# Kernel optimization log

Measured on AMD Instinct MI355X. Metric: run time of the kernel, lower is better.

## Reference

```python
import math
import jax, jax.numpy as jnp
import numpy as np

B, T, C = 2, 2048, 1024
H, HKV, HD = 16, 4, 64  # n_head, n_kv_head, head_dim
G = H // HKV            # GQA groups
WS = 1024               # sliding window size
GATE_CH = 32


def setup_inputs() -> dict:
    key = jax.random.key(0)
    ks = jax.random.split(key, 8)
    x = jax.random.normal(ks[0], (B, T, C), dtype=jnp.float32)
    ve = jax.random.normal(ks[1], (B, T, HKV * HD), dtype=jnp.float32)
    # realistic RoPE tables: half head_dim frequencies
    d = HD // 2
    inv_freq = 1.0 / (10000.0 ** (jnp.arange(d, dtype=jnp.float32) / d))
    angles = jnp.arange(T, dtype=jnp.float32)[:, None] * inv_freq[None, :]  # (T, d)
    cos = jnp.cos(angles)[None, :, None, :]  # (1, T, 1, d)
    sin = jnp.sin(angles)[None, :, None, :]
    s = 0.02
    Wq = s * jax.random.normal(ks[2], (C, H * HD), dtype=jnp.float32)
    Wk = s * jax.random.normal(ks[3], (C, HKV * HD), dtype=jnp.float32)
    Wv = s * jax.random.normal(ks[4], (C, HKV * HD), dtype=jnp.float32)
    Wproj = s * jax.random.normal(ks[5], (C, C), dtype=jnp.float32)
    Wg = s * jax.random.normal(ks[6], (GATE_CH, HKV), dtype=jnp.float32)
    return {"x": x, "ve": ve, "cos": cos, "sin": sin,
            "Wq": Wq, "Wk": Wk, "Wv": Wv, "Wproj": Wproj, "Wg": Wg, "ws": WS}


def _rope(u, cos, sin):
    d = u.shape[-1] // 2
    u1, u2 = u[..., :d], u[..., d:]
    return jnp.concatenate([u1 * cos + u2 * sin, -u1 * sin + u2 * cos], axis=-1)


def _rmsnorm(u):
    eps = jnp.finfo(u.dtype).eps
    return u * jax.lax.rsqrt(jnp.mean(u * u, axis=-1, keepdims=True) + eps)


def reference(x, ve, cos, sin, Wq, Wk, Wv, Wproj, Wg, ws):
    b, t, c = x.shape
    q = (x @ Wq).reshape(b, t, H, HD)
    k = (x @ Wk).reshape(b, t, HKV, HD)
    v = (x @ Wv).reshape(b, t, HKV, HD)
    # value-embedding gate: 2*sigmoid over first 32 channels of x
    gate = 2.0 * jax.nn.sigmoid(x[..., :GATE_CH] @ Wg)  # (b, t, HKV)
    v = v + gate[..., None] * ve.reshape(b, t, HKV, HD)
    q = _rmsnorm(_rope(q, cos, sin))
    k = _rmsnorm(_rope(k, cos, sin))
    # GQA: view q as (b, t, HKV, G, HD), contract against shared k/v per kv-head
    qg = q.reshape(b, t, HKV, G, HD)
    scale = 1.0 / math.sqrt(HD)
    scores = jnp.einsum('bqhgd,bkhd->bhgqk', qg, k) * scale  # (b, HKV, G, t, t)
    pos = jnp.arange(t)
    # key j attends iff i - ws + 1 <= j <= i (sliding causal window)
    mask = (pos[None, :] >= pos[:, None] - ws + 1) & (pos[None, :] <= pos[:, None])
    scores = jnp.where(mask[None, None, None], scores, -jnp.inf)
    attn = jax.nn.softmax(scores, axis=-1)
    y = jnp.einsum('bhgqk,bkhd->bqhgd', attn, v).reshape(b, t, H * HD)
    return y @ Wproj
```

## Files before the change

kernel.cpp:

```cpp
#include <hip/hip_runtime.h>
#include <hip/hip_bf16.h>

#define Bq 2
#define Tq 2048
#define Cq 1024
#define Hq 16
#define HKVq 4
#define HDq 64
#define Gq 4
#define WSq 1024
#define GATE_CHq 32

typedef __attribute__((ext_vector_type(8))) short short8;
typedef __attribute__((ext_vector_type(4))) float f32x4;
typedef __attribute__((ext_vector_type(2))) unsigned int u32x2;
typedef unsigned int u32;
typedef unsigned short u16;

#if __has_builtin(__builtin_amdgcn_exp2f)
#define EXP2(x) __builtin_amdgcn_exp2f(x)
#else
#define EXP2(x) exp2f(x)
#endif

__device__ __forceinline__ u16 f2bf(float f) {
  u32 u = __float_as_uint(f);
  u32 r = (u + 0x7FFFu + ((u >> 16) & 1u)) >> 16;
  return (u16)r;
}
__device__ __forceinline__ float bf2f(u16 u) {
  return __uint_as_float(((u32)u) << 16);
}

__device__ __forceinline__ void gl_lds16(const u16* g, u16* l) {
  __builtin_amdgcn_global_load_lds(
      (const u32 __attribute__((address_space(1)))*)g,
      (u32 __attribute__((address_space(3)))*)l, 16, 0, 0);
}

__global__ __launch_bounds__(256) void qkv_gemm_fused(
    const u16* __restrict__ A, const u16* __restrict__ Bt,
    const float* __restrict__ ve, const float* __restrict__ cosp,
    const float* __restrict__ sinp, const float* __restrict__ gatebuf,
    u16* __restrict__ Qb, u16* __restrict__ Kb, u16* __restrict__ Vtb) {
  __shared__ __attribute__((aligned(16))) u16 As[64 * 64];
  __shared__ __attribute__((aligned(16))) u16 Bs[128 * 64];

  const int bx = blockIdx.x;
  const int bm0 = blockIdx.y * 64, bn0 = bx * 128;
  const int tid = threadIdx.x;
  const int w = tid >> 6, lane = tid & 63;
  const int wm = (w >> 1) * 32, wn = (w & 1) * 64;
  const int quad = lane >> 4, l16 = lane & 15;
  const int K = 1024;

  f32x4 acc[2][4];
#pragma unroll
  for (int mt = 0; mt < 2; mt++)
#pragma unroll
    for (int nt = 0; nt < 4; nt++) acc[mt][nt] = (f32x4){0.f, 0.f, 0.f, 0.f};

  int goffA[2], goffB[4];
#pragma unroll
  for (int i = 0; i < 2; i++) {
    int s = i * 256 + tid;
    int m = s >> 3, gp = s & 7;
    goffA[i] = m * K + (gp ^ (m & 7)) * 8;
  }
#pragma unroll
  for (int i = 0; i < 4; i++) {
    int s = i * 256 + tid;
    int m = s >> 3, gp = s & 7;
    goffB[i] = m * K + (gp ^ (m & 7)) * 8;
  }
  const u16* Ab = A + (long)bm0 * K;
  const u16* Bb = Bt + (long)bn0 * K;

  for (int k0 = 0; k0 < K; k0 += 64) {
    __syncthreads();
#pragma unroll
    for (int i = 0; i < 2; i++)
      gl_lds16(Ab + goffA[i] + k0, &As[(i * 256 + w * 64) * 8]);
#pragma unroll
    for (int i = 0; i < 4; i++)
      gl_lds16(Bb + goffB[i] + k0, &Bs[(i * 256 + w * 64) * 8]);
    __syncthreads();

#pragma unroll
    for (int ks = 0; ks < 2; ks++) {
      short8 af[2], bf[4];
#pragma unroll
      for (int mt = 0; mt < 2; mt++) {
        int ml = wm + mt * 16 + l16;
        af[mt] = *(const short8*)&As[ml * 64 + (((ks * 4 + quad) ^ (ml & 7)) * 8)];
      }
#pragma unroll
      for (int nt = 0; nt < 4; nt++) {
        int nl = wn + nt * 16 + l16;
        bf[nt] = *(const short8*)&Bs[nl * 64 + (((ks * 4 + quad) ^ (nl & 7)) * 8)];
      }
#pragma unroll
      for (int mt = 0; mt < 2; mt++)
#pragma unroll
        for (int nt = 0; nt < 4; nt++)
          acc[mt][nt] = __builtin_amdgcn_mfma_f32_16x16x32_bf16(
              af[mt], bf[nt], acc[mt][nt], 0, 0, 0);
    }
  }

  const int b = bm0 >> 11;
  const int tseq0 = (bm0 & 2047) + wm;

  if (bx < 10) {
    u16* Dst;
    if (bx < 8) {
      int hh = bx * 2 + (w & 1);
      int hkv = hh >> 2, g = hh & 3;
      Dst = Qb + ((long)((b * 4 + hkv) * 4 + g) * Tq) * 64;
    } else {
      int kk = (bx - 8) * 2 + (w & 1);
      Dst = Kb + ((long)(b * 4 + kk) * Tq) * 64;
    }
#pragma unroll
    for (int mt = 0; mt < 2; mt++) {
#pragma unroll
      for (int r = 0; r < 4; r++) {
        int t = tseq0 + mt * 16 + quad * 4 + r;
        float c0 = cosp[t * 32 + l16];
        float s0 = sinp[t * 32 + l16];
        float c1 = cosp[t * 32 + 16 + l16];
        float s1 = sinp[t * 32 + 16 + l16];
        float a0 = acc[mt][0][r], a1 = acc[mt][1][r];
        float a2 = acc[mt][2][r], a3 = acc[mt][3][r];
        float rp0 = a0 * c0 + a2 * s0;
        float rp1 = a1 * c1 + a3 * s1;
        float rp2 = a2 * c0 - a0 * s0;
        float rp3 = a3 * c1 - a1 * s1;
        float ss = rp0 * rp0 + rp1 * rp1 + rp2 * rp2 + rp3 * rp3;
        ss += __shfl_xor(ss, 1);
        ss += __shfl_xor(ss, 2);
        ss += __shfl_xor(ss, 4);
        ss += __shfl_xor(ss, 8);
        float sc = rsqrtf(ss * (1.f / 64.f) + 1.1920928955078125e-07f);
        u16* drow = Dst + (long)t * 64;
        drow[l16] = f2bf(rp0 * sc);
        drow[16 + l16] = f2bf(rp1 * sc);
        drow[32 + l16] = f2bf(rp2 * sc);
        drow[48 + l16] = f2bf(rp3 * sc);
      }
    }
  } else {
    int kk = (bx - 10) * 2 + (w & 1);
    u16* Dst = Vtb + ((long)(b * 4 + kk) * 64) * Tq;
#pragma unroll
    for (int mt = 0; mt < 2; mt++) {
      float vals[4][4];
#pragma unroll
      for (int r = 0; r < 4; r++) {
        int t = tseq0 + mt * 16 + quad * 4 + r;
        long bt = (long)b * Tq + t;
        float gv = gatebuf[bt * 4 + kk];
        const float* verow = ve + bt * 256 + kk * 64;
#pragma unroll
        for (int nt = 0; nt < 4; nt++)
          vals[nt][r] = acc[mt][nt][r] + gv * verow[nt * 16 + l16];
      }
      int t0m = tseq0 + mt * 16 + quad * 4;
#pragma unroll
      for (int nt = 0; nt < 4; nt++) {
        int d = nt * 16 + l16;
        union { short4 v; u16 u[4]; } p;
#pragma unroll
        for (int r = 0; r < 4; r++) p.u[r] = f2bf(vals[nt][r]);
        *(short4*)(Dst + (long)d * Tq + t0m) = p.v;
      }
    }
  }
}

__global__ __launch_bounds__(256) void gemm_proj(
    const u16* __restrict__ A, const u16* __restrict__ Bt,
    float* __restrict__ C, int M, int N, int K) {
  __shared__ __attribute__((aligned(16))) u16 As[64 * 64];
  __shared__ __attribute__((aligned(16))) u16 Bs[128 * 64];

  const int bm0 = blockIdx.y * 64, bn0 = blockIdx.x * 128;
  const int tid = threadIdx.x;
  const int w = tid >> 6, lane = tid & 63;
  const int wm = (w >> 1) * 32, wn = (w & 1) * 64;
  const int quad = lane >> 4, l16 = lane & 15;

  f32x4 acc[2][4];
#pragma unroll
  for (int mt = 0; mt < 2; mt++)
#pragma unroll
    for (int nt = 0; nt < 4; nt++) acc[mt][nt] = (f32x4){0.f, 0.f, 0.f, 0.f};

  int goffA[2], goffB[4];
#pragma unroll
  for (int i = 0; i < 2; i++) {
    int s = i * 256 + tid;
    int m = s >> 3, gp = s & 7;
    goffA[i] = m * K + (gp ^ (m & 7)) * 8;
  }
#pragma unroll
  for (int i = 0; i < 4; i++) {
    int s = i * 256 + tid;
    int m = s >> 3, gp = s & 7;
    goffB[i] = m * K + (gp ^ (m & 7)) * 8;
  }
  const u16* Ab = A + (long)bm0 * K;
  const u16* Bb = Bt + (long)bn0 * K;

  for (int k0 = 0; k0 < K; k0 += 64) {
    __syncthreads();
#pragma unroll
    for (int i = 0; i < 2; i++)
      gl_lds16(Ab + goffA[i] + k0, &As[(i * 256 + w * 64) * 8]);
#pragma unroll
    for (int i = 0; i < 4; i++)
      gl_lds16(Bb + goffB[i] + k0, &Bs[(i * 256 + w * 64) * 8]);
    __syncthreads();

#pragma unroll
    for (int ks = 0; ks < 2; ks++) {
      short8 af[2], bf[4];
#pragma unroll
      for (int mt = 0; mt < 2; mt++) {
        int ml = wm + mt * 16 + l16;
        af[mt] = *(const short8*)&As[ml * 64 + (((ks * 4 + quad) ^ (ml & 7)) * 8)];
      }
#pragma unroll
      for (int nt = 0; nt < 4; nt++) {
        int nl = wn + nt * 16 + l16;
        bf[nt] = *(const short8*)&Bs[nl * 64 + (((ks * 4 + quad) ^ (nl & 7)) * 8)];
      }
#pragma unroll
      for (int mt = 0; mt < 2; mt++)
#pragma unroll
        for (int nt = 0; nt < 4; nt++)
          acc[mt][nt] = __builtin_amdgcn_mfma_f32_16x16x32_bf16(
              af[mt], bf[nt], acc[mt][nt], 0, 0, 0);
    }
  }

#pragma unroll
  for (int mt = 0; mt < 2; mt++)
#pragma unroll
    for (int nt = 0; nt < 4; nt++) {
      int row0 = bm0 + wm + mt * 16 + quad * 4;
      int col = bn0 + wn + nt * 16 + l16;
#pragma unroll
      for (int r = 0; r < 4; r++)
        C[(long)(row0 + r) * N + col] = acc[mt][nt][r];
    }
}

__global__ __launch_bounds__(256) void prep(
    const float* __restrict__ x, u16* __restrict__ xb,
    const float* __restrict__ Wq, const float* __restrict__ Wk,
    const float* __restrict__ Wv, const float* __restrict__ Wproj,
    const float* __restrict__ Wg, u16* __restrict__ Dqkv,
    u16* __restrict__ Dproj, float* __restrict__ gatebuf) {
  __shared__ float tile[64][65];
  int bx = blockIdx.x;
  int tid = threadIdx.x;
  if (bx < 2048) {
    int i = (bx * 256 + tid) * 8;
    float4 a = *(const float4*)(x + i);
    float4 b = *(const float4*)(x + i + 4);
    union { short8 v; u16 u[8]; } o;
    o.u[0] = f2bf(a.x); o.u[1] = f2bf(a.y); o.u[2] = f2bf(a.z); o.u[3] = f2bf(a.w);
    o.u[4] = f2bf(b.x); o.u[5] = f2bf(b.y); o.u[6] = f2bf(b.z); o.u[7] = f2bf(b.w);
    *(short8*)(xb + i) = o.v;
    return;
  }
  if (bx >= 2688) {
    int p = (bx - 2688) * 256 + tid;
    int bt = p >> 2, kk = p & 3;
    const float* xr = x + (long)bt * Cq;
    float dot = 0.f;
#pragma unroll
    for (int i = 0; i < GATE_CHq; i++) dot += xr[i] * Wg[i * HKVq + kk];
    gatebuf[p] = 2.f / (1.f + expf(-dot));
    return;
  }
  int wb = bx - 2048;
  int obx = wb >> 4;
  int k0 = (wb & 15) * 64;
  const float* S;
  u16* Dst;
  int N, nb;
  if (obx < 16)      { S = Wq;    N = 1024; nb = obx;      Dst = Dqkv; }
  else if (obx < 20) { S = Wk;    N = 256;  nb = obx - 16; Dst = Dqkv + 1024 * 1024; }
  else if (obx < 24) { S = Wv;    N = 256;  nb = obx - 20; Dst = Dqkv + 1280 * 1024; }
  else               { S = Wproj; N = 1024; nb = obx - 24; Dst = Dproj; }
  int n0 = nb * 64;
#pragma unroll
  for (int i = 0; i < 16; i++) {
    int idx = i * 256 + tid;
    int kl = idx >> 6, nl = idx & 63;
    tile[kl][nl] = S[(long)(k0 + kl) * N + n0 + nl];
  }
  __syncthreads();
#pragma unroll
  for (int i = 0; i < 16; i++) {
    int idx = i * 256 + tid;
    int nl = idx >> 6, kl = idx & 63;
    Dst[(long)(n0 + nl) * 1024 + k0 + kl] = f2bf(tile[kl][nl]);
  }
}

#define CEXP 0.18033688011112042f
#define CEXP8 1.4426950408889634f

template <bool MASK>
__device__ __forceinline__ void attn_half(
    int k0h, int key_base, int vg_base, int q0, int quad, int l16,
    const u16* __restrict__ Ks, const u16* __restrict__ Vts,
    u32* __restrict__ myPs, const short8 (&QB)[2][2], f32x4 (&O)[2][4],
    float (&lsum)[2]) {
  f32x4 S4[4][2];
#pragma unroll
  for (int kt4 = 0; kt4 < 4; kt4++) {
    int key = key_base + kt4 * 16 + l16;
    short8 kb0 = *(const short8*)(&Ks[key * 64 + ((quad ^ (key & 7)) * 8)]);
    short8 kb1 = *(const short8*)(&Ks[key * 64 + (((4 + quad) ^ (key & 7)) * 8)]);
#pragma unroll
    for (int qj = 0; qj < 2; qj++) {
      f32x4 acc = (f32x4){0.f, 0.f, 0.f, 0.f};
      acc = __builtin_amdgcn_mfma_f32_16x16x32_bf16(kb0, QB[qj][0], acc, 0, 0, 0);
      acc = __builtin_amdgcn_mfma_f32_16x16x32_bf16(kb1, QB[qj][1], acc, 0, 0, 0);
      S4[kt4][qj] = acc;
    }
  }

#pragma unroll
  for (int kt4 = 0; kt4 < 4; kt4++)
#pragma unroll
    for (int qj = 0; qj < 2; qj++) {
      float Pv[4];
#pragma unroll
      for (int r = 0; r < 4; r++) {
        float sv = S4[kt4][qj][r];
        if (MASK) {
          int kpos = k0h + kt4 * 16 + quad * 4 + r;
          int qpos = q0 + qj * 16 + l16;
          bool valid = (kpos <= qpos) && (kpos >= qpos - (WSq - 1));
          sv = valid ? sv : -1e30f;
        }
        float p = EXP2(__builtin_fmaf(sv, CEXP, -CEXP8));
        Pv[r] = p;
        lsum[qj] += p;
      }
      u32x2 pk;
#pragma unroll
      for (int rp = 0; rp < 2; rp++) {
        u32 lo = __float_as_uint(Pv[2 * rp]) + 0x8000u;
        u32 hi = __float_as_uint(Pv[2 * rp + 1]) + 0x8000u;
        pk[rp] = __builtin_amdgcn_perm(hi, lo, 0x07060302u);
      }
      *(u32x2*)(&myPs[(qj * 16 + l16) * 36 + kt4 * 8 + quad * 2]) = pk;
    }

  short8 vb[4][2];
#pragma unroll
  for (int nt = 0; nt < 4; nt++) {
    int d = nt * 16 + l16;
    vb[nt][0] = *(const short8*)(&Vts[d * 128 + (((vg_base + quad) ^ (d & 7)) * 8)]);
    vb[nt][1] =
        *(const short8*)(&Vts[d * 128 + (((vg_base + 4 + quad) ^ (d & 7)) * 8)]);
  }

#pragma unroll
  for (int qj = 0; qj < 2; qj++) {
    const u32* prow = &myPs[(qj * 16 + l16) * 36];
    short8 pa0 = *(const short8*)(prow + quad * 4);
    short8 pa1 = *(const short8*)(prow + 16 + quad * 4);
#pragma unroll
    for (int nt = 0; nt < 4; nt++) {
      O[qj][nt] =
          __builtin_amdgcn_mfma_f32_16x16x32_bf16(pa0, vb[nt][0], O[qj][nt], 0, 0, 0);
      O[qj][nt] =
          __builtin_amdgcn_mfma_f32_16x16x32_bf16(pa1, vb[nt][1], O[qj][nt], 0, 0, 0);
    }
  }
}

__global__ __launch_bounds__(256, 2) void attn_mfma(
    const u16* __restrict__ Qb, const u16* __restrict__ Kb,
    const u16* __restrict__ Vtb, u16* __restrict__ Yb) {
  __shared__ __attribute__((aligned(16))) u16 Ks[128 * 64];
  __shared__ __attribute__((aligned(16))) u16 Vts[64 * 128];
  __shared__ __attribute__((aligned(16))) u32 Ps[4][2][32 * 36];

  int bid = blockIdx.x;
  int bh = bid & 7;
  int qt32 = bid >> 3;
  int hkv = bh & 3;
  int b = bh >> 2;
  int q0 = qt32 * 32;
  int tid = threadIdx.x;
  int g = tid >> 6;
  int lane = tid & 63;
  int quad = lane >> 4;
  int l16 = lane & 15;

  short8 QB[2][2];
#pragma unroll
  for (int qj = 0; qj < 2; qj++) {
    const u16* qb =
        Qb + ((long)((bh * 4 + g) * Tq + q0 + qj * 16 + l16)) * 64 + quad * 8;
    QB[qj][0] = *(const short8*)(qb);
    QB[qj][1] = *(const short8*)(qb + 32);
  }

  f32x4 O[2][4];
#pragma unroll
  for (int qj = 0; qj < 2; qj++)
#pragma unroll
    for (int nt = 0; nt < 4; nt++) O[qj][nt] = (f32x4){0.f, 0.f, 0.f, 0.f};
  float lsum[2] = {0.f, 0.f};

  int lo = q0 - (WSq - 1);
  int st = (lo < 0 ? 0 : lo) >> 7;
  int et = (q0 + 31) >> 7;

  const u16* Kbase = Kb + ((long)bh * Tq) * 64;
  const u16* Vbase = Vtb + ((long)bh * 64) * Tq;

  int rowoffK[4], rowoffV[4];
#pragma unroll
  for (int i = 0; i < 4; i++) {
    int s = i * 256 + tid;
    int kr = s >> 3, kgp = s & 7;
    rowoffK[i] = kr * 64 + (kgp ^ (kr & 7)) * 8;
    int d = s >> 4, vgp = s & 15;
    rowoffV[i] = d * Tq + (vgp ^ (d & 7)) * 8;
  }

  for (int kt = st; kt <= et; kt++) {
    int k0 = kt << 7;
    __syncthreads();
#pragma unroll
    for (int i = 0; i < 4; i++) {
      gl_lds16(Kbase + (long)k0 * 64 + rowoffK[i], &Ks[(i * 256 + g * 64) * 8]);
      gl_lds16(Vbase + k0 + rowoffV[i], &Vts[(i * 256 + g * 64) * 8]);
    }
    __syncthreads();

    bool needC = (k0 + 127 > q0);
    bool needW = (k0 < q0 - 992);
    if (needC || needW) {
      attn_half<true>(k0, 0, 0, q0, quad, l16, Ks, Vts, &Ps[g][0][0], QB, O, lsum);
      attn_half<true>(k0 + 64, 64, 8, q0, quad, l16, Ks, Vts, &Ps[g][1][0], QB,
                      O, lsum);
    } else {
      attn_half<false>(k0, 0, 0, q0, quad, l16, Ks, Vts, &Ps[g][0][0], QB, O,
                       lsum);
      attn_half<false>(k0 + 64, 64, 8, q0, quad, l16, Ks, Vts, &Ps[g][1][0], QB,
                       O, lsum);
    }
  }

#pragma unroll
  for (int qj = 0; qj < 2; qj++) {
    lsum[qj] += __shfl_xor(lsum[qj], 16);
    lsum[qj] += __shfl_xor(lsum[qj], 32);
  }

  int h = hkv * 4 + g;
#pragma unroll
  for (int qj = 0; qj < 2; qj++) {
    float invl[4];
#pragma unroll
    for (int r = 0; r < 4; r++) invl[r] = 1.f / __shfl(lsum[qj], quad * 4 + r);
#pragma unroll
    for (int nt = 0; nt < 4; nt++)
#pragma unroll
      for (int r = 0; r < 4; r++)
        Yb[((long)(b * Tq + q0 + qj * 16 + quad * 4 + r)) * 1024 + h * 64 +
           nt * 16 + l16] = f2bf(O[qj][nt][r] * invl[r]);
  }
}

extern "C" void kernel_launch(void* const* d_in, const int* in_sizes, int n_in,
                              void* d_out, int out_size, void* d_ws,
                              size_t ws_size, hipStream_t stream) {
  const float* x     = (const float*)d_in[0];
  const float* ve    = (const float*)d_in[1];
  const float* cosp  = (const float*)d_in[2];
  const float* sinp  = (const float*)d_in[3];
  const float* Wq    = (const float*)d_in[4];
  const float* Wk    = (const float*)d_in[5];
  const float* Wv    = (const float*)d_in[6];
  const float* Wproj = (const float*)d_in[7];
  const float* Wg    = (const float*)d_in[8];

  char* base = (char*)d_ws;
  u16* xb      = (u16*)(base);
  u16* Yb      = xb;
  u16* WqkvT   = (u16*)(base + 8388608);
  u16* WprojT  = (u16*)(base + 11534336);
  u16* Qb      = (u16*)(base + 13631488);
  u16* Kb      = (u16*)(base + 22020096);
  u16* Vtb     = (u16*)(base + 24117248);
  float* gateb = (float*)(base + 26214400);
  float* out = (float*)d_out;

  prep<<<2752, 256, 0, stream>>>(x, xb, Wq, Wk, Wv, Wproj, Wg, WqkvT, WprojT,
                                 gateb);
  qkv_gemm_fused<<<dim3(12, 64), 256, 0, stream>>>(xb, WqkvT, ve, cosp, sinp,
                                                   gateb, Qb, Kb, Vtb);
  attn_mfma<<<512, 256, 0, stream>>>(Qb, Kb, Vtb, Yb);
  gemm_proj<<<dim3(8, 64), 256, 0, stream>>>(Yb, WprojT, out, 4096, 1024, 1024);
}
```

Baseline: 162.0 us.

## Switch attention to 32x32x16 MFMA with register-resident P and double-buffered K/V

Rewrites the attention inner tile around 32x32x16 bf16 MFMA with S^T layout. The softmax probabilities are packed and redistributed across lanes with permlane32_swap instead of a round trip through LDS, which removes the Ps scratch buffer. K/V tiles are double-buffered in LDS so the next tile's global-to-LDS load overlaps compute, dropping one barrier per iteration. The output is stored as 4-element vectors. Together these aim to cut LDS traffic and synchronisation stalls, at the cost of twice the K/V LDS footprint and higher register pressure from the 16-wide accumulators.

```diff
diff --git a/kernel.cpp b/kernel.cpp
--- a/kernel.cpp
+++ b/kernel.cpp
@@ -13,6 +13,7 @@
 
 typedef __attribute__((ext_vector_type(8))) short short8;
 typedef __attribute__((ext_vector_type(4))) float f32x4;
+typedef __attribute__((ext_vector_type(16))) float f32x16;
 typedef __attribute__((ext_vector_type(2))) unsigned int u32x2;
 typedef unsigned int u32;
 typedef unsigned short u16;
@@ -315,74 +316,60 @@
 #define CEXP8 1.4426950408889634f
 
 template <bool MASK>
-__device__ __forceinline__ void attn_half(
-    int k0h, int key_base, int vg_base, int q0, int quad, int l16,
-    const u16* __restrict__ Ks, const u16* __restrict__ Vts,
-    u32* __restrict__ myPs, const short8 (&QB)[2][2], f32x4 (&O)[2][4],
-    float (&lsum)[2]) {
-  f32x4 S4[4][2];
-#pragma unroll
-  for (int kt4 = 0; kt4 < 4; kt4++) {
-    int key = key_base + kt4 * 16 + l16;
-    short8 kb0 = *(const short8*)(&Ks[key * 64 + ((quad ^ (key & 7)) * 8)]);
-    short8 kb1 = *(const short8*)(&Ks[key * 64 + (((4 + quad) ^ (key & 7)) * 8)]);
-#pragma unroll
-    for (int qj = 0; qj < 2; qj++) {
-      f32x4 acc = (f32x4){0.f, 0.f, 0.f, 0.f};
-      acc = __builtin_amdgcn_mfma_f32_16x16x32_bf16(kb0, QB[qj][0], acc, 0, 0, 0);
-      acc = __builtin_amdgcn_mfma_f32_16x16x32_bf16(kb1, QB[qj][1], acc, 0, 0, 0);
-      S4[kt4][qj] = acc;
-    }
-  }
-
-#pragma unroll
-  for (int kt4 = 0; kt4 < 4; kt4++)
-#pragma unroll
-    for (int qj = 0; qj < 2; qj++) {
-      float Pv[4];
-#pragma unroll
-      for (int r = 0; r < 4; r++) {
-        float sv = S4[kt4][qj][r];
-        if (MASK) {
-          int kpos = k0h + kt4 * 16 + quad * 4 + r;
-          int qpos = q0 + qj * 16 + l16;
-          bool valid = (kpos <= qpos) && (kpos >= qpos - (WSq - 1));
-          sv = valid ? sv : -1e30f;
-        }
-        float p = EXP2(__builtin_fmaf(sv, CEXP, -CEXP8));
-        Pv[r] = p;
-        lsum[qj] += p;
-      }
-      u32x2 pk;
-#pragma unroll
-      for (int rp = 0; rp < 2; rp++) {
-        u32 lo = __float_as_uint(Pv[2 * rp]) + 0x8000u;
-        u32 hi = __float_as_uint(Pv[2 * rp + 1]) + 0x8000u;
-        pk[rp] = __builtin_amdgcn_perm(hi, lo, 0x07060302u);
-      }
-      *(u32x2*)(&myPs[(qj * 16 + l16) * 36 + kt4 * 8 + quad * 2]) = pk;
-    }
-
-  short8 vb[4][2];
-#pragma unroll
-  for (int nt = 0; nt < 4; nt++) {
-    int d = nt * 16 + l16;
-    vb[nt][0] = *(const short8*)(&Vts[d * 128 + (((vg_base + quad) ^ (d & 7)) * 8)]);
-    vb[nt][1] =
-        *(const short8*)(&Vts[d * 128 + (((vg_base + 4 + quad) ^ (d & 7)) * 8)]);
-  }
-
-#pragma unroll
-  for (int qj = 0; qj < 2; qj++) {
-    const u32* prow = &myPs[(qj * 16 + l16) * 36];
-    short8 pa0 = *(const short8*)(prow + quad * 4);
-    short8 pa1 = *(const short8*)(prow + 16 + quad * 4);
-#pragma unroll
-    for (int nt = 0; nt < 4; nt++) {
-      O[qj][nt] =
-          __builtin_amdgcn_mfma_f32_16x16x32_bf16(pa0, vb[nt][0], O[qj][nt], 0, 0, 0);
-      O[qj][nt] =
-          __builtin_amdgcn_mfma_f32_16x16x32_bf16(pa1, vb[nt][1], O[qj][nt], 0, 0, 0);
+__device__ __forceinline__ void attn_tile32(
+    int k0, int q0, int l31, int hl, const u16* __restrict__ Ks,
+    const u16* __restrict__ Vts, const short8 (&QB)[4], f32x16& O0, f32x16& O1,
+    float& lsum) {
+  const int qpos = q0 + l31;
+#pragma unroll
+  for (int c = 0; c < 4; c++) {
+    const int key = c * 32 + l31;
+    f32x16 S;
+#pragma unroll
+    for (int i = 0; i < 16; i++) S[i] = 0.f;
+#pragma unroll
+    for (int s = 0; s < 4; s++) {
+      short8 kf = *(const short8*)&Ks[key * 64 + (((s * 2 + hl) ^ (key & 7)) * 8)];
+      S = __builtin_amdgcn_mfma_f32_32x32x16_bf16(kf, QB[s], S, 0, 0, 0);
+    }
+    const int kb = k0 + c * 32 + 4 * hl;
+    float p[16];
+#pragma unroll
+    for (int r = 0; r < 16; r++) {
+      float sv = S[r];
+      if (MASK) {
+        int kpos = kb + (r & 3) + 8 * (r >> 2);
+        u32 diff = (u32)(qpos - kpos);
+        sv = (diff < (u32)WSq) ? sv : -1e30f;
+      }
+      float pv = EXP2(__builtin_fmaf(sv, CEXP, -CEXP8));
+      lsum += pv;
+      p[r] = pv;
+    }
+    u32 w[8];
+#pragma unroll
+    for (int i = 0; i < 8; i++) {
+      u32 lo = __float_as_uint(p[2 * i]) + 0x8000u;
+      u32 hi = __float_as_uint(p[2 * i + 1]) + 0x8000u;
+      w[i] = __builtin_amdgcn_perm(hi, lo, 0x07060302u);
+    }
+    u32x2 r02 = __builtin_amdgcn_permlane32_swap(w[0], w[2], false, false);
+    u32x2 r13 = __builtin_amdgcn_permlane32_swap(w[1], w[3], false, false);
+    u32x2 r46 = __builtin_amdgcn_permlane32_swap(w[4], w[6], false, false);
+    u32x2 r57 = __builtin_amdgcn_permlane32_swap(w[5], w[7], false, false);
+    union { short8 s8; u32 u[4]; } f0, f1;
+    f0.u[0] = r02[0]; f0.u[1] = r13[0]; f0.u[2] = r02[1]; f0.u[3] = r13[1];
+    f1.u[0] = r46[0]; f1.u[1] = r57[0]; f1.u[2] = r46[1]; f1.u[3] = r57[1];
+    const int d0 = l31, d1 = 32 + l31;
+    const int sw = (l31 & 7);
+#pragma unroll
+    for (int kc = 0; kc < 2; kc++) {
+      int grp = c * 4 + kc * 2 + hl;
+      short8 v0 = *(const short8*)&Vts[d0 * 128 + ((grp ^ sw) * 8)];
+      short8 v1 = *(const short8*)&Vts[d1 * 128 + ((grp ^ sw) * 8)];
+      const short8 pf = kc ? f1.s8 : f0.s8;
+      O0 = __builtin_amdgcn_mfma_f32_32x32x16_bf16(v0, pf, O0, 0, 0, 0);
+      O1 = __builtin_amdgcn_mfma_f32_32x32x16_bf16(v1, pf, O1, 0, 0, 0);
     }
   }
 }
@@ -390,9 +377,8 @@
 __global__ __launch_bounds__(256, 2) void attn_mfma(
     const u16* __restrict__ Qb, const u16* __restrict__ Kb,
     const u16* __restrict__ Vtb, u16* __restrict__ Yb) {
-  __shared__ __attribute__((aligned(16))) u16 Ks[128 * 64];
-  __shared__ __attribute__((aligned(16))) u16 Vts[64 * 128];
-  __shared__ __attribute__((aligned(16))) u32 Ps[4][2][32 * 36];
+  __shared__ __attribute__((aligned(16))) u16 Ks[2][128 * 64];
+  __shared__ __attribute__((aligned(16))) u16 Vts[2][64 * 128];
 
   int bid = blockIdx.x;
   int bh = bid & 7;
@@ -403,24 +389,21 @@
   int tid = threadIdx.x;
   int g = tid >> 6;
   int lane = tid & 63;
-  int quad = lane >> 4;
-  int l16 = lane & 15;
-
-  short8 QB[2][2];
-#pragma unroll
-  for (int qj = 0; qj < 2; qj++) {
+  int l31 = lane & 31;
+  int hl = lane >> 5;
+
+  short8 QB[4];
+  {
     const u16* qb =
-        Qb + ((long)((bh * 4 + g) * Tq + q0 + qj * 16 + l16)) * 64 + quad * 8;
-    QB[qj][0] = *(const short8*)(qb);
-    QB[qj][1] = *(const short8*)(qb + 32);
-  }
-
-  f32x4 O[2][4];
-#pragma unroll
-  for (int qj = 0; qj < 2; qj++)
-#pragma unroll
-    for (int nt = 0; nt < 4; nt++) O[qj][nt] = (f32x4){0.f, 0.f, 0.f, 0.f};
-  float lsum[2] = {0.f, 0.f};
+        Qb + ((long)((bh * 4 + g) * Tq + q0 + l31)) * 64 + hl * 8;
+#pragma unroll
+    for (int s = 0; s < 4; s++) QB[s] = *(const short8*)(qb + s * 16);
+  }
+
+  f32x16 O0, O1;
+#pragma unroll
+  for (int i = 0; i < 16; i++) { O0[i] = 0.f; O1[i] = 0.f; }
+  float lsum = 0.f;
 
   int lo = q0 - (WSq - 1);
   int st = (lo < 0 ? 0 : lo) >> 7;
@@ -439,48 +422,56 @@
     rowoffV[i] = d * Tq + (vgp ^ (d & 7)) * 8;
   }
 
+  {
+    int k0 = st << 7;
+#pragma unroll
+    for (int i = 0; i < 4; i++) {
+      gl_lds16(Kbase + (long)k0 * 64 + rowoffK[i], &Ks[0][(i * 256 + g * 64) * 8]);
+      gl_lds16(Vbase + k0 + rowoffV[i], &Vts[0][(i * 256 + g * 64) * 8]);
+    }
+  }
+  __syncthreads();
+
+  int cur = 0;
   for (int kt = st; kt <= et; kt++) {
     int k0 = kt << 7;
-    __syncthreads();
-#pragma unroll
-    for (int i = 0; i < 4; i++) {
-      gl_lds16(Kbase + (long)k0 * 64 + rowoffK[i], &Ks[(i * 256 + g * 64) * 8]);
-      gl_lds16(Vbase + k0 + rowoffV[i], &Vts[(i * 256 + g * 64) * 8]);
-    }
-    __syncthreads();
-
+    if (kt < et) {
+      int k0n = k0 + 128;
+#pragma unroll
+      for (int i = 0; i < 4; i++) {
+        gl_lds16(Kbase + (long)k0n * 64 + rowoffK[i],
+                 &Ks[cur ^ 1][(i * 256 + g * 64) * 8]);
+        gl_lds16(Vbase + k0n + rowoffV[i],
+                 &Vts[cur ^ 1][(i * 256 + g * 64) * 8]);
+      }
+    }
     bool needC = (k0 + 127 > q0);
     bool needW = (k0 < q0 - 992);
     if (needC || needW) {
-      attn_half<true>(k0, 0, 0, q0, quad, l16, Ks, Vts, &Ps[g][0][0], QB, O, lsum);
-      attn_half<true>(k0 + 64, 64, 8, q0, quad, l16, Ks, Vts, &Ps[g][1][0], QB,
-                      O, lsum);
+      attn_tile32<true>(k0, q0, l31, hl, Ks[cur], Vts[cur], QB, O0, O1, lsum);
     } else {
-      attn_half<false>(k0, 0, 0, q0, quad, l16, Ks, Vts, &Ps[g][0][0], QB, O,
-                       lsum);
-      attn_half<false>(k0 + 64, 64, 8, q0, quad, l16, Ks, Vts, &Ps[g][1][0], QB,
-                       O, lsum);
-    }
-  }
-
-#pragma unroll
-  for (int qj = 0; qj < 2; qj++) {
-    lsum[qj] += __shfl_xor(lsum[qj], 16);
-    lsum[qj] += __shfl_xor(lsum[qj], 32);
-  }
+      attn_tile32<false>(k0, q0, l31, hl, Ks[cur], Vts[cur], QB, O0, O1, lsum);
+    }
+    __syncthreads();
+    cur ^= 1;
+  }
+
+  lsum += __shfl_xor(lsum, 32);
+  float invl = 1.f / lsum;
 
   int h = hkv * 4 + g;
-#pragma unroll
-  for (int qj = 0; qj < 2; qj++) {
-    float invl[4];
-#pragma unroll
-    for (int r = 0; r < 4; r++) invl[r] = 1.f / __shfl(lsum[qj], quad * 4 + r);
-#pragma unroll
-    for (int nt = 0; nt < 4; nt++)
-#pragma unroll
-      for (int r = 0; r < 4; r++)
-        Yb[((long)(b * Tq + q0 + qj * 16 + quad * 4 + r)) * 1024 + h * 64 +
-           nt * 16 + l16] = f2bf(O[qj][nt][r] * invl[r]);
+  u16* yrow = Yb + ((long)(b * Tq + q0 + l31)) * 1024 + h * 64;
+#pragma unroll
+  for (int g4 = 0; g4 < 4; g4++) {
+    union { short4 v; u16 u[4]; } pk0, pk1;
+#pragma unroll
+    for (int i = 0; i < 4; i++) {
+      pk0.u[i] = f2bf(O0[g4 * 4 + i] * invl);
+      pk1.u[i] = f2bf(O1[g4 * 4 + i] * invl);
+    }
+    int dA = 8 * g4 + 4 * hl;
+    *(short4*)(yrow + dA) = pk0.v;
+    *(short4*)(yrow + 32 + dA) = pk1.v;
   }
 }
 
```

Measured after the change: 162.7 us. Within noise of the previous version (+0.5%).
